# Performance work log

Measured on AMD Instinct MI355X. Metric: run time of the kernel, lower is better.

Reference implementation:

```python
import jax, jax.numpy as jnp
import numpy as np

BN_EPS = 1e-5


def setup_inputs() -> dict:
    key = jax.random.key(0)
    ks = jax.random.split(key, 8)
    b, c, h, w, d = 16, 256, 128, 128, 64
    x = jax.random.normal(ks[0], (b, c, h, w), dtype=jnp.float32)
    conv1_w = jax.random.normal(ks[1], (c, c), dtype=jnp.float32) * np.sqrt(2.0 / c)
    conv1_b = jax.random.normal(ks[2], (c,), dtype=jnp.float32) * 0.02
    mk_w = jax.random.normal(ks[3], (d, c), dtype=jnp.float32) * np.sqrt(2.0 / d)
    mv_w = jnp.transpose(mk_w)  # original ties mv.weight = mk.weight.permute(1,0,2)
    conv2_w = jax.random.normal(ks[4], (c, c), dtype=jnp.float32) * np.sqrt(2.0 / c)
    bn_gamma = jnp.ones((c,), dtype=jnp.float32)
    bn_beta = jnp.zeros((c,), dtype=jnp.float32)
    bn_mean = jax.random.normal(ks[5], (c,), dtype=jnp.float32) * 0.1
    bn_var = jax.random.uniform(ks[6], (c,), dtype=jnp.float32, minval=0.5, maxval=1.5)
    return {"x": x, "conv1_w": conv1_w, "conv1_b": conv1_b, "mk_w": mk_w,
            "mv_w": mv_w, "conv2_w": conv2_w, "bn_gamma": bn_gamma,
            "bn_beta": bn_beta, "bn_mean": bn_mean, "bn_var": bn_var}


def reference(x, conv1_w, conv1_b, mk_w, mv_w, conv2_w, bn_gamma, bn_beta, bn_mean, bn_var):
    b, c, h, w = x.shape
    n = h * w
    identity = x
    # conv1: 1x1 conv with bias -> [b, c, n]
    y = jnp.einsum('oc,bchw->bohw', conv1_w, x) + conv1_b[None, :, None, None]
    y = y.reshape(b, c, n)
    # external attention: mk projection [b, d, n]
    attn = jnp.einsum('dc,bcn->bdn', mk_w, y)
    attn = jax.nn.softmax(attn, axis=-1)              # softmax over spatial N
    attn = attn / (1e-9 + attn.sum(axis=1, keepdims=True))  # column-normalize over d
    # mv projection back to channels [b, c, n]
    z = jnp.einsum('cd,bdn->bcn', mv_w, attn)
    z = z.reshape(b, c, h, w)
    # conv2 (1x1, no bias) + BatchNorm (inference) + residual + relu
    z = jnp.einsum('oc,bchw->bohw', conv2_w, z)
    inv = bn_gamma / jnp.sqrt(bn_var + BN_EPS)
    z = z * inv[None, :, None, None] + (bn_beta - bn_mean * inv)[None, :, None, None]
    return jax.nn.relu(z + identity)
```

## Files before the change

### kernel.cpp

```cpp
#include <hip/hip_runtime.h>
#include <hip/hip_bf16.h>

#define HW 16384
#define C  256
#define D  64
#define NB 16
#define M0 16.0f
#define LOG2E 1.44269504088896340736f

typedef unsigned short u16;
typedef __attribute__((ext_vector_type(4))) float  f32x4;
typedef __attribute__((ext_vector_type(4))) short  s16x4;
typedef __attribute__((ext_vector_type(8))) short  s16x8;

__device__ __forceinline__ float bf2f(u16 u) {
    return __uint_as_float(((unsigned int)u) << 16);
}
__device__ __forceinline__ short f2bfs(float f) {
    union { __hip_bfloat16 h; short s; } u;
    u.h = __float2bfloat16(f);
    return u.s;
}
__device__ __forceinline__ u16 f2bf(float f) {
    unsigned int u = __float_as_uint(f);
    unsigned int r = (u + 0x7fffu + ((u >> 16) & 1u)) >> 16;
    return (u16)r;
}

#define MFMA16(a, b, c) __builtin_amdgcn_mfma_f32_16x16x32_bf16((a), (b), (c), 0, 0, 0)

__global__ void precompute_kernel(const float* __restrict__ conv1_w,
                                  const float* __restrict__ conv1_b,
                                  const float* __restrict__ mk_w,
                                  const float* __restrict__ mv_w,
                                  const float* __restrict__ conv2_w,
                                  const float* __restrict__ gamma,
                                  const float* __restrict__ beta,
                                  const float* __restrict__ mean,
                                  const float* __restrict__ var,
                                  short* __restrict__ Ath,
                                  short* __restrict__ Atl,
                                  float* __restrict__ amk,
                                  short* __restrict__ Bmb,
                                  float* __restrict__ shift,
                                  float* __restrict__ esum)
{
    int gid = blockIdx.x * blockDim.x + threadIdx.x;
    if (gid < C * D) {
        int d = gid >> 8, cp = gid & 255;
        float s = 0.f;
        for (int c = 0; c < C; ++c) s += mk_w[d * C + c] * conv1_w[c * C + cp];
        u16 h = f2bf(s);
        Ath[gid] = (short)h;
        Atl[gid] = (short)f2bf(s - bf2f(h));
    } else if (gid < 2 * C * D) {
        int g = gid - C * D;
        int o = g >> 6, d = g & 63;
        float inv = gamma[o] * rsqrtf(var[o] + 1e-5f);
        float s = 0.f;
        for (int c = 0; c < C; ++c) s += conv2_w[o * C + c] * mv_w[c * D + d];
        Bmb[g] = (short)f2bf(s * inv);
    } else if (gid < 2 * C * D + D) {
        int d = gid - 2 * C * D;
        float s = 0.f;
        for (int c = 0; c < C; ++c) s += mk_w[d * C + c] * conv1_b[c];
        amk[d] = s;
    } else if (gid < 2 * C * D + D + C) {
        int o = gid - (2 * C * D + D);
        float inv = gamma[o] * rsqrtf(var[o] + 1e-5f);
        shift[o] = beta[o] - mean[o] * inv;
    } else if (gid < 2 * C * D + D + C + NB * D) {
        esum[gid - (2 * C * D + D + C)] = 0.f;
    }
}

#define NT1 64
#define CH  128
#define XR1 (CH + 8)
__global__ __launch_bounds__(256, 5) void pexp_kernel(const float* __restrict__ x,
                                                      const short* __restrict__ Ath,
                                                      const short* __restrict__ Atl,
                                                      const float* __restrict__ amk,
                                                      u16* __restrict__ pexp,
                                                      float* __restrict__ esum)
{
    __shared__ short xs[NT1 * XR1];
    const int t = threadIdx.x;
    const int b = blockIdx.y;
    const int n0 = blockIdx.x * NT1;
    const int lane = t & 63, w = t >> 6;
    const int col = lane & 15, g = lane >> 4;

    const float* xb = x + (size_t)b * C * HW + n0;

    f32x4 zz = {0.f, 0.f, 0.f, 0.f};
    f32x4 acc[4] = { zz, zz, zz, zz };

    for (int h = 0; h < 2; ++h) {
        const int ch = h * CH;
        if (h) __syncthreads();

        #pragma unroll
        for (int i = 0; i < 2; ++i) {
            int cell = i * 256 + t;
            int nq = cell & 15, cq = cell >> 4;
            int c0 = cq * 4, nn = nq * 4;
            const float* gp = xb + (size_t)(ch + c0) * HW + nn;
            f32x4 r0 = *(const f32x4*)(gp);
            f32x4 r1 = *(const f32x4*)(gp + HW);
            f32x4 r2 = *(const f32x4*)(gp + 2 * HW);
            f32x4 r3 = *(const f32x4*)(gp + 3 * HW);
            #pragma unroll
            for (int j = 0; j < 4; ++j) {
                s16x4 hi = { f2bfs(r0[j]), f2bfs(r1[j]), f2bfs(r2[j]), f2bfs(r3[j]) };
                *(s16x4*)&xs[(nn + j) * XR1 + c0] = hi;
            }
        }

        s16x8 Ah[4], Al[4];
        {
            const short* ah = Ath + (size_t)(w * 16 + col) * C + ch + 8 * g;
            const short* al = Atl + (size_t)(w * 16 + col) * C + ch + 8 * g;
            #pragma unroll
            for (int ks = 0; ks < 4; ++ks) {
                Ah[ks] = *(const s16x8*)(ah + ks * 32);
                Al[ks] = *(const s16x8*)(al + ks * 32);
            }
        }
        __syncthreads();

        #pragma unroll
        for (int ks = 0; ks < 4; ++ks) {
            #pragma unroll
            for (int nt = 0; nt < 4; ++nt) {
                s16x8 xf = *(const s16x8*)&xs[(nt * 16 + col) * XR1 + ks * 32 + 8 * g];
                acc[nt] = MFMA16(xf, Ah[ks], acc[nt]);
                acc[nt] = MFMA16(xf, Al[ks], acc[nt]);
            }
        }
    }

    const float am = amk[w * 16 + col];
    u16* pb = pexp + (size_t)b * D * HW + (size_t)(w * 16 + col) * HW + n0;
    float rs = 0.f;
    #pragma unroll
    for (int nt = 0; nt < 4; ++nt) {
        s16x4 st4;
        #pragma unroll
        for (int r = 0; r < 4; ++r) {
            float e = exp2f((acc[nt][r] + am - M0) * LOG2E);
            rs += e;
            st4[r] = f2bfs(e);
        }
        *(s16x4*)(pb + nt * 16 + 4 * g) = st4;
    }
    rs += __shfl_xor(rs, 16);
    rs += __shfl_xor(rs, 32);
    if (lane < 16) atomicAdd(esum + b * D + w * 16 + lane, rs);
}

#define NT3 64
__global__ __launch_bounds__(256, 3) void out_kernel(const float* __restrict__ x,
                                                     const u16* __restrict__ pexp,
                                                     const float* __restrict__ esum,
                                                     const short* __restrict__ Bmb,
                                                     const float* __restrict__ shift,
                                                     float* __restrict__ out)
{
    __shared__ short ps[NT3 * 72];
    __shared__ float csum[4][NT3];
    __shared__ float rr[NT3];

    const int t = threadIdx.x;
    const int b  = (NB - 1) - blockIdx.y;
    const int n0 = ((int)gridDim.x - 1 - blockIdx.x) * NT3;

    {
        const int nl = t & 63, dq = t >> 6;
        const u16* lg = pexp + (size_t)b * D * HW + (size_t)(dq * 16) * HW + n0 + nl;
        const float* es = esum + b * D + dq * 16;
        float cs = 0.f;
        #pragma unroll
        for (int j4 = 0; j4 < 4; ++j4) {
            s16x4 pk;
            #pragma unroll
            for (int jj = 0; jj < 4; ++jj) {
                int j = j4 * 4 + jj;
                float iv = __fdividef(1.0f, es[j]);
                float pv = bf2f(lg[(size_t)j * HW]) * iv;
                cs += pv;
                pk[jj] = f2bfs(pv);
            }
            *(s16x4*)&ps[nl * 72 + dq * 16 + j4 * 4] = pk;
        }
        csum[dq][nl] = cs;
    }
    __syncthreads();
    if (t < NT3)
        rr[t] = __fdividef(1.0f, csum[0][t] + csum[1][t] + csum[2][t] + csum[3][t] + 1e-9f);
    __syncthreads();

    const int lane = t & 63, col = lane & 15, g = lane >> 4;
    const int w = t >> 6;

    s16x8 Bf[4][2];
    #pragma unroll
    for (int ot = 0; ot < 4; ++ot) {
        const short* bp = Bmb + (size_t)(w * 64 + ot * 16 + col) * D + 8 * g;
        Bf[ot][0] = *(const s16x8*)(bp);
        Bf[ot][1] = *(const s16x8*)(bp + 32);
    }

    f32x4 zz = {0.f, 0.f, 0.f, 0.f};
    f32x4 acc[4][4];
    #pragma unroll
    for (int ot = 0; ot < 4; ++ot)
        #pragma unroll
        for (int nt = 0; nt < 4; ++nt) acc[ot][nt] = zz;

    #pragma unroll
    for (int nt = 0; nt < 4; ++nt) {
        const short* pr = &ps[(nt * 16 + col) * 72 + 8 * g];
        s16x8 p0 = *(const s16x8*)(pr);
        s16x8 p1 = *(const s16x8*)(pr + 32);
        #pragma unroll
        for (int ot = 0; ot < 4; ++ot) {
            acc[ot][nt] = MFMA16(p0, Bf[ot][0], acc[ot][nt]);
            acc[ot][nt] = MFMA16(p1, Bf[ot][1], acc[ot][nt]);
        }
    }

    float sh[4];
    #pragma unroll
    for (int ot = 0; ot < 4; ++ot) sh[ot] = shift[w * 64 + ot * 16 + col];

    const float* xb = x + (size_t)b * C * HW + n0;
    float* ob = out + (size_t)b * C * HW + n0;
    #pragma unroll
    for (int nt = 0; nt < 4; ++nt) {
        f32x4 rv = *(const f32x4*)&rr[nt * 16 + 4 * g];
        #pragma unroll
        for (int ot = 0; ot < 4; ++ot) {
            const size_t off = (size_t)(w * 64 + ot * 16 + col) * HW + nt * 16 + 4 * g;
            f32x4 xv = *(const f32x4*)(xb + off);
            f32x4 vv;
            #pragma unroll
            for (int r = 0; r < 4; ++r)
                vv[r] = fmaxf(acc[ot][nt][r] * rv[r] + sh[ot] + xv[r], 0.f);
            __builtin_nontemporal_store(vv, (f32x4*)(ob + off));
        }
    }
}

extern "C" void kernel_launch(void* const* d_in, const int* in_sizes, int n_in,
                              void* d_out, int out_size, void* d_ws, size_t ws_size,
                              hipStream_t stream)
{
    const float* x       = (const float*)d_in[0];
    const float* conv1_w = (const float*)d_in[1];
    const float* conv1_b = (const float*)d_in[2];
    const float* mk_w    = (const float*)d_in[3];
    const float* mv_w    = (const float*)d_in[4];
    const float* conv2_w = (const float*)d_in[5];
    const float* gamma   = (const float*)d_in[6];
    const float* beta    = (const float*)d_in[7];
    const float* mean    = (const float*)d_in[8];
    const float* var     = (const float*)d_in[9];
    float* out = (float*)d_out;

    float* amk   = (float*)d_ws;
    float* shift = amk + D;
    float* esum  = shift + C;
    short* Ath   = (short*)(esum + NB * D);
    short* Atl   = Ath + C * D;
    short* Bmb   = Atl + C * D;
    u16* pexp    = (u16*)(Bmb + C * D);

    const int pre_work = 2 * C * D + D + C + NB * D;
    precompute_kernel<<<(pre_work + 255) / 256, 256, 0, stream>>>(
        conv1_w, conv1_b, mk_w, mv_w, conv2_w, gamma, beta, mean, var,
        Ath, Atl, amk, Bmb, shift, esum);

    pexp_kernel<<<dim3(HW / NT1, NB), 256, 0, stream>>>(x, Ath, Atl, amk, pexp, esum);

    out_kernel<<<dim3(HW / NT3, NB), 256, 0, stream>>>(x, pexp, esum, Bmb, shift, out);
}
```

Baseline: 544.5 us.

## Widen spatial tiles in pexp and out kernels, split out_kernel channels over grid

pexp_kernel now handles 128 spatial positions per block and walks channels in four 64-wide chunks, giving each wave eight accumulator tiles and reusing the A fragments across more columns. out_kernel takes 128-position tiles and splits the 256 output channels into two halves over a new grid dimension. Each wave covers a 64x64 output subtile, and the reciprocal esum values are computed once per block into shared memory. The aim is more reuse per block and less per-element division, at the cost of lower occupancy in pexp and recomputing the normalized P tile in both channel halves.

```diff
diff --git a/kernel.cpp b/kernel.cpp
--- a/kernel.cpp
+++ b/kernel.cpp
@@ -74,10 +74,10 @@
     }
 }
 
-#define NT1 64
-#define CH  128
-#define XR1 (CH + 8)
-__global__ __launch_bounds__(256, 5) void pexp_kernel(const float* __restrict__ x,
+#define NT1 128
+#define CQ  64
+#define XR1 72
+__global__ __launch_bounds__(256, 4) void pexp_kernel(const float* __restrict__ x,
                                                       const short* __restrict__ Ath,
                                                       const short* __restrict__ Atl,
                                                       const float* __restrict__ amk,
@@ -94,16 +94,16 @@
     const float* xb = x + (size_t)b * C * HW + n0;
 
     f32x4 zz = {0.f, 0.f, 0.f, 0.f};
-    f32x4 acc[4] = { zz, zz, zz, zz };
-
-    for (int h = 0; h < 2; ++h) {
-        const int ch = h * CH;
-        if (h) __syncthreads();
+    f32x4 acc[8] = { zz, zz, zz, zz, zz, zz, zz, zz };
+
+    for (int q = 0; q < 4; ++q) {
+        const int ch = q * CQ;
+        if (q) __syncthreads();
 
         #pragma unroll
         for (int i = 0; i < 2; ++i) {
             int cell = i * 256 + t;
-            int nq = cell & 15, cq = cell >> 4;
+            int nq = cell & 31, cq = cell >> 5;
             int c0 = cq * 4, nn = nq * 4;
             const float* gp = xb + (size_t)(ch + c0) * HW + nn;
             f32x4 r0 = *(const f32x4*)(gp);
@@ -117,12 +117,12 @@
             }
         }
 
-        s16x8 Ah[4], Al[4];
+        s16x8 Ah[2], Al[2];
         {
             const short* ah = Ath + (size_t)(w * 16 + col) * C + ch + 8 * g;
             const short* al = Atl + (size_t)(w * 16 + col) * C + ch + 8 * g;
             #pragma unroll
-            for (int ks = 0; ks < 4; ++ks) {
+            for (int ks = 0; ks < 2; ++ks) {
                 Ah[ks] = *(const s16x8*)(ah + ks * 32);
                 Al[ks] = *(const s16x8*)(al + ks * 32);
             }
@@ -130,9 +130,9 @@
         __syncthreads();
 
         #pragma unroll
-        for (int ks = 0; ks < 4; ++ks) {
-            #pragma unroll
-            for (int nt = 0; nt < 4; ++nt) {
+        for (int ks = 0; ks < 2; ++ks) {
+            #pragma unroll
+            for (int nt = 0; nt < 8; ++nt) {
                 s16x8 xf = *(const s16x8*)&xs[(nt * 16 + col) * XR1 + ks * 32 + 8 * g];
                 acc[nt] = MFMA16(xf, Ah[ks], acc[nt]);
                 acc[nt] = MFMA16(xf, Al[ks], acc[nt]);
@@ -144,7 +144,7 @@
     u16* pb = pexp + (size_t)b * D * HW + (size_t)(w * 16 + col) * HW + n0;
     float rs = 0.f;
     #pragma unroll
-    for (int nt = 0; nt < 4; ++nt) {
+    for (int nt = 0; nt < 8; ++nt) {
         s16x4 st4;
         #pragma unroll
         for (int r = 0; r < 4; ++r) {
@@ -159,7 +159,8 @@
     if (lane < 16) atomicAdd(esum + b * D + w * 16 + lane, rs);
 }
 
-#define NT3 64
+#define NT3 128
+#define PR3 72
 __global__ __launch_bounds__(256, 3) void out_kernel(const float* __restrict__ x,
                                                      const u16* __restrict__ pexp,
                                                      const float* __restrict__ esum,
@@ -167,46 +168,51 @@
                                                      const float* __restrict__ shift,
                                                      float* __restrict__ out)
 {
-    __shared__ short ps[NT3 * 72];
-    __shared__ float csum[4][NT3];
+    __shared__ short ps[NT3 * PR3];
+    __shared__ float csum[2][NT3];
     __shared__ float rr[NT3];
+    __shared__ float einv[D];
 
     const int t = threadIdx.x;
-    const int b  = (NB - 1) - blockIdx.y;
-    const int n0 = ((int)gridDim.x - 1 - blockIdx.x) * NT3;
+    const int b  = (NB - 1) - (int)blockIdx.z;
+    const int oh = blockIdx.y;
+    const int n0 = ((int)gridDim.x - 1 - (int)blockIdx.x) * NT3;
+
+    if (t < D) einv[t] = __fdividef(1.0f, esum[b * D + t]);
+    __syncthreads();
 
     {
-        const int nl = t & 63, dq = t >> 6;
-        const u16* lg = pexp + (size_t)b * D * HW + (size_t)(dq * 16) * HW + n0 + nl;
-        const float* es = esum + b * D + dq * 16;
+        const int nl = t & 127, dh = t >> 7;
+        const u16* lg = pexp + (size_t)b * D * HW + (size_t)(dh * 32) * HW + n0 + nl;
         float cs = 0.f;
         #pragma unroll
-        for (int j4 = 0; j4 < 4; ++j4) {
+        for (int j4 = 0; j4 < 8; ++j4) {
             s16x4 pk;
             #pragma unroll
             for (int jj = 0; jj < 4; ++jj) {
                 int j = j4 * 4 + jj;
-                float iv = __fdividef(1.0f, es[j]);
-                float pv = bf2f(lg[(size_t)j * HW]) * iv;
+                float pv = bf2f(lg[(size_t)j * HW]) * einv[dh * 32 + j];
                 cs += pv;
                 pk[jj] = f2bfs(pv);
             }
-            *(s16x4*)&ps[nl * 72 + dq * 16 + j4 * 4] = pk;
-        }
-        csum[dq][nl] = cs;
+            *(s16x4*)&ps[nl * PR3 + dh * 32 + j4 * 4] = pk;
+        }
+        csum[dh][nl] = cs;
     }
     __syncthreads();
     if (t < NT3)
-        rr[t] = __fdividef(1.0f, csum[0][t] + csum[1][t] + csum[2][t] + csum[3][t] + 1e-9f);
+        rr[t] = __fdividef(1.0f, csum[0][t] + csum[1][t] + 1e-9f);
     __syncthreads();
 
     const int lane = t & 63, col = lane & 15, g = lane >> 4;
     const int w = t >> 6;
+    const int obase = oh * 128 + (w >> 1) * 64;
+    const int nb = (w & 1) * 64;
 
     s16x8 Bf[4][2];
     #pragma unroll
     for (int ot = 0; ot < 4; ++ot) {
-        const short* bp = Bmb + (size_t)(w * 64 + ot * 16 + col) * D + 8 * g;
+        const short* bp = Bmb + (size_t)(obase + ot * 16 + col) * D + 8 * g;
         Bf[ot][0] = *(const s16x8*)(bp);
         Bf[ot][1] = *(const s16x8*)(bp + 32);
     }
@@ -220,7 +226,7 @@
 
     #pragma unroll
     for (int nt = 0; nt < 4; ++nt) {
-        const short* pr = &ps[(nt * 16 + col) * 72 + 8 * g];
+        const short* pr = &ps[(nb + nt * 16 + col) * PR3 + 8 * g];
         s16x8 p0 = *(const s16x8*)(pr);
         s16x8 p1 = *(const s16x8*)(pr + 32);
         #pragma unroll
@@ -232,16 +238,16 @@
 
     float sh[4];
     #pragma unroll
-    for (int ot = 0; ot < 4; ++ot) sh[ot] = shift[w * 64 + ot * 16 + col];
+    for (int ot = 0; ot < 4; ++ot) sh[ot] = shift[obase + ot * 16 + col];
 
     const float* xb = x + (size_t)b * C * HW + n0;
     float* ob = out + (size_t)b * C * HW + n0;
     #pragma unroll
     for (int nt = 0; nt < 4; ++nt) {
-        f32x4 rv = *(const f32x4*)&rr[nt * 16 + 4 * g];
+        f32x4 rv = *(const f32x4*)&rr[nb + nt * 16 + 4 * g];
         #pragma unroll
         for (int ot = 0; ot < 4; ++ot) {
-            const size_t off = (size_t)(w * 64 + ot * 16 + col) * HW + nt * 16 + 4 * g;
+            const size_t off = (size_t)(obase + ot * 16 + col) * HW + nb + nt * 16 + 4 * g;
             f32x4 xv = *(const f32x4*)(xb + off);
             f32x4 vv;
             #pragma unroll
@@ -283,5 +289,5 @@
 
     pexp_kernel<<<dim3(HW / NT1, NB), 256, 0, stream>>>(x, Ath, Atl, amk, pexp, esum);
 
-    out_kernel<<<dim3(HW / NT3, NB), 256, 0, stream>>>(x, pexp, esum, Bmb, shift, out);
-}
+    out_kernel<<<dim3(HW / NT3, 2, NB), 256, 0, stream>>>(x, pexp, esum, Bmb, shift, out);
+}
```

After: 545.3 us. About the same (+0.1%).
